# Kernel tuning notes

Measured on AMD Instinct MI355X. Metric: run time of the kernel, lower is better.

## Reference

```python
import jax, jax.numpy as jnp
import numpy as np

E = 1024   # embedding_size
K = 64     # key_size
DH = 64    # head_size
H = 16     # layer_size (num heads)
F = 4096   # hidden_size
B, S = 4, 2048
EPS = float(np.finfo(np.float32).eps)  # torch RMSNorm default eps


def setup_inputs() -> dict:
    key = jax.random.key(0)
    ks = jax.random.split(key, 12)
    embeddings = jax.random.normal(ks[0], (B, S, E), dtype=jnp.float32)
    # causal additive mask: 0 on/below diagonal, -1e9 above
    tri = jnp.triu(jnp.ones((S, S), dtype=bool), k=1)
    causal_buffer = jnp.where(tri, -1e9, 0.0).astype(jnp.float32)[None]  # [1,S,S]
    # standard RoPE cos/sin buffers over the key dim
    inv_freq = 1.0 / (10000.0 ** (jnp.arange(0, K // 2, dtype=jnp.float32) * 2.0 / K))
    ang = jnp.arange(S, dtype=jnp.float32)[:, None] * inv_freq[None, :]  # [S,K/2]
    ang = jnp.concatenate([ang, ang], axis=-1)                           # [S,K]
    cos_buffer = jnp.cos(ang)[None]  # [1,S,K]
    sin_buffer = jnp.sin(ang)[None]
    sc = 0.02
    wq = jax.random.normal(ks[1], (H, E, K), dtype=jnp.float32) * sc
    wk = jax.random.normal(ks[2], (H, E, K), dtype=jnp.float32) * sc
    wv = jax.random.normal(ks[3], (H, E, DH), dtype=jnp.float32) * sc
    w_proj = jax.random.normal(ks[4], (E, E), dtype=jnp.float32) * sc
    attn_norm_w = jnp.ones((E,), dtype=jnp.float32)
    mlp_norm_w = jnp.ones((E,), dtype=jnp.float32)
    w_up = jax.random.normal(ks[5], (E, F), dtype=jnp.float32) * sc
    w_gate = jax.random.normal(ks[6], (E, F), dtype=jnp.float32) * sc
    w_down = jax.random.normal(ks[7], (F, E), dtype=jnp.float32) * sc
    return {"embeddings": embeddings, "causal_buffer": causal_buffer,
            "cos_buffer": cos_buffer, "sin_buffer": sin_buffer,
            "wq": wq, "wk": wk, "wv": wv, "w_proj": w_proj,
            "attn_norm_w": attn_norm_w, "mlp_norm_w": mlp_norm_w,
            "w_up": w_up, "w_gate": w_gate, "w_down": w_down}


def _rmsnorm(x, w):
    ms = jnp.mean(x * x, axis=-1, keepdims=True)
    return x * jax.lax.rsqrt(ms + EPS) * w


def _rotate(x, cos, sin):
    # x: [B,H,S,K]; cos/sin: [1,1,S,K]. swapped = cat(second_half, first_half)
    swapped = jnp.concatenate([x[..., K // 2:], x[..., :K // 2]], axis=-1)
    return cos * x + sin * swapped


def reference(embeddings, causal_buffer, cos_buffer, sin_buffer,
              wq, wk, wv, w_proj, attn_norm_w, mlp_norm_w,
              w_up, w_gate, w_down):
    cos = cos_buffer[:, None]  # [1,1,S,K]
    sin = sin_buffer[:, None]
    # NOTE: original computes attention_norm(embeddings) but feeds RAW
    # embeddings to the heads; we reproduce that faithfully.
    q = _rotate(jnp.einsum('bse,hek->bhsk', embeddings, wq), cos, sin)
    k = _rotate(jnp.einsum('bse,hek->bhsk', embeddings, wk), cos, sin)
    v = jnp.einsum('bse,hed->bhsd', embeddings, wv)
    scores = jnp.einsum('bhsk,bhtk->bhst', q, k) / jnp.sqrt(jnp.float32(K))
    scores = scores + causal_buffer[:, None]  # broadcast over heads
    weights = jax.nn.softmax(scores, axis=-1)
    attn = jnp.einsum('bhst,bhtd->bhsd', weights, v)  # [B,H,S,DH]
    attn = attn.transpose(0, 2, 1, 3).reshape(attn.shape[0], attn.shape[2], H * DH)
    x = embeddings + attn @ w_proj
    h = _rmsnorm(x, mlp_norm_w)
    mlp = (h @ w_up) * jax.nn.elu(h @ w_gate)
    return x + mlp @ w_down
```

## Files before the change

### kernel.cpp

```cpp
#include <hip/hip_runtime.h>
#include <cstdint>
#include <cstddef>

#define E_DIM 1024
#define S_LEN 2048
#define NB 4
#define NH 16
#define F_DIM 4096

typedef __attribute__((ext_vector_type(8))) __bf16 bf16x8;
typedef __attribute__((ext_vector_type(4))) __bf16 bf16x4;
typedef __attribute__((ext_vector_type(4))) float f32x4;

__device__ __forceinline__ f32x4 mfma16(bf16x8 a, bf16x8 b, f32x4 c) {
  return __builtin_amdgcn_mfma_f32_16x16x32_bf16(a, b, c, 0, 0, 0);
}

__device__ __forceinline__ unsigned short f2bf(float f) {
  __bf16 h = (__bf16)f;
  return __builtin_bit_cast(unsigned short, h);
}

__device__ __forceinline__ void gl_lds16(const void* gptr, void* lptr) {
  __builtin_amdgcn_global_load_lds(
      (const __attribute__((address_space(1))) void*)gptr,
      (__attribute__((address_space(3))) void*)lptr, 16, 0, 0);
}


__global__ __launch_bounds__(256) void cast_emb_kernel(
    const float4* __restrict__ in, ushort4* __restrict__ out) {
  int i = blockIdx.x * 256 + threadIdx.x;
  float4 v = in[i];
  ushort4 o;
  o.x = f2bf(v.x); o.y = f2bf(v.y); o.z = f2bf(v.z); o.w = f2bf(v.w);
  out[i] = o;
}

__global__ __launch_bounds__(256) void transpose_cast_kernel(
    const float* __restrict__ in, unsigned short* __restrict__ out, int R, int C) {
  __shared__ float tile[32][33];
  const int bz = blockIdx.z;
  const float* ip = in + (size_t)bz * R * C;
  const int r0 = blockIdx.y * 32, c0 = blockIdx.x * 32;
  const int tc = threadIdx.x & 31, tr = threadIdx.x >> 5;
#pragma unroll
  for (int i = 0; i < 4; ++i)
    tile[tr + i * 8][tc] = ip[(size_t)(r0 + tr + i * 8) * C + (c0 + tc)];
  __syncthreads();
#pragma unroll
  for (int i = 0; i < 4; ++i)
    out[(size_t)(bz * C + c0 + tr + i * 8) * R + (r0 + tc)] = f2bf(tile[tc][tr + i * 8]);
}

template <int EPI>
__global__ __launch_bounds__(256) void gemm_bt(
    const unsigned short* __restrict__ A, const unsigned short* __restrict__ Bt,
    int Kd, int N,
    const float* __restrict__ aux, const float* __restrict__ cosb,
    const float* __restrict__ sinb,
    unsigned short* __restrict__ qout, unsigned short* __restrict__ kout,
    unsigned short* __restrict__ vtout, float* __restrict__ fout) {
  __shared__ unsigned short As[128 * 64];
  __shared__ unsigned short Bs[128 * 64];
  const int t = threadIdx.x;
  const int lane = t & 63, w = t >> 6;
  const int quad = lane >> 4, l15 = lane & 15;
  const int wm = (w >> 1) * 64, wn = (w & 1) * 64;
  const int m0 = blockIdx.y * 128, n0 = blockIdx.x * 128;
  const int sr = t >> 3, sc = t & 7;
  const int gcoff = (sc ^ (sr & 7)) * 8;
  const unsigned short* ga = A + (size_t)(m0 + sr) * Kd + gcoff;
  const unsigned short* gb = Bt + (size_t)(n0 + sr) * Kd + gcoff;
  unsigned short* lA = &As[sr * 64 + sc * 8];
  unsigned short* lB = &Bs[sr * 64 + sc * 8];
  const int xh = l15 & 7;
  f32x4 acc[4][4] = {};
  for (int k0 = 0; k0 < Kd; k0 += 64) {
    __syncthreads();
#pragma unroll
    for (int i = 0; i < 4; ++i) {
      gl_lds16(ga + (size_t)(i * 32) * Kd + k0, lA + i * 32 * 64);
      gl_lds16(gb + (size_t)(i * 32) * Kd + k0, lB + i * 32 * 64);
    }
    __syncthreads();
#pragma unroll
    for (int ks = 0; ks < 2; ++ks) {
      bf16x8 af[4], bfr[4];
#pragma unroll
      for (int mi = 0; mi < 4; ++mi)
        af[mi] = *reinterpret_cast<const bf16x8*>(
            &As[(wm + mi * 16 + l15) * 64 + (((ks * 4 + quad) ^ xh) * 8)]);
#pragma unroll
      for (int ni = 0; ni < 4; ++ni)
        bfr[ni] = *reinterpret_cast<const bf16x8*>(
            &Bs[(wn + ni * 16 + l15) * 64 + (((ks * 4 + quad) ^ xh) * 8)]);
#pragma unroll
      for (int mi = 0; mi < 4; ++mi)
#pragma unroll
        for (int ni = 0; ni < 4; ++ni)
          acc[mi][ni] = mfma16(af[mi], bfr[ni], acc[mi][ni]);
    }
  }
  if (EPI == 0) {
#pragma unroll
    for (int mi = 0; mi < 4; ++mi) {
      const int mbase = m0 + wm + mi * 16 + quad * 4;
#pragma unroll
      for (int nt = 0; nt < 4; ++nt) {
        const int n = n0 + wn + nt * 16 + l15;
        const int seg = n >> 10, rest = n & 1023, hh = rest >> 6, kk = rest & 63;
#pragma unroll
        for (int rg = 0; rg < 4; ++rg) {
          const int m = mbase + rg;
          const int b = m >> 11, s = m & 2047;
          const float v = acc[mi][nt][rg];
          if (seg == 2) {
            vtout[(((size_t)(b * NH + hh)) * 64 + kk) * S_LEN + s] = f2bf(v);
          } else {
            const float sw = acc[mi][nt ^ 2][rg];
            const float cv = cosb[s * 64 + kk], sv = sinb[s * 64 + kk];
            const float scl = (seg == 0) ? 0.125f : 1.0f;
            unsigned short* dst = (seg == 0) ? qout : kout;
            dst[(((size_t)(b * NH + hh)) * S_LEN + s) * 64 + kk] = f2bf((cv * v + sv * sw) * scl);
          }
        }
      }
    }
  } else {
#pragma unroll
    for (int mi = 0; mi < 4; ++mi) {
      const int mbase = m0 + wm + mi * 16 + quad * 4;
#pragma unroll
      for (int nt = 0; nt < 4; ++nt) {
        const int n = n0 + wn + nt * 16 + l15;
#pragma unroll
        for (int rg = 0; rg < 4; ++rg) {
          const size_t idx = (size_t)(mbase + rg) * 1024 + n;
          fout[idx] = aux[idx] + acc[mi][nt][rg];
        }
      }
    }
  }
}

__global__ __launch_bounds__(256) void gemm_upgate(
    const unsigned short* __restrict__ A, const unsigned short* __restrict__ Bu,
    const unsigned short* __restrict__ Bg, unsigned short* __restrict__ gout) {
  __shared__ unsigned short As[128 * 64];
  __shared__ unsigned short Us[64 * 64];
  __shared__ unsigned short Gs[64 * 64];
  const int Kd = 1024;
  const int t = threadIdx.x;
  const int lane = t & 63, w = t >> 6;
  const int quad = lane >> 4, l15 = lane & 15;
  const int wm = (w >> 1) * 64, wn = (w & 1) * 32;
  const int m0 = blockIdx.y * 128, n0 = blockIdx.x * 64;
  const int sr = t >> 3, sc = t & 7;
  const int gcoff = (sc ^ (sr & 7)) * 8;
  const unsigned short* ga = A + (size_t)(m0 + sr) * Kd + gcoff;
  const unsigned short* gu = Bu + (size_t)(n0 + sr) * Kd + gcoff;
  const unsigned short* gg = Bg + (size_t)(n0 + sr) * Kd + gcoff;
  unsigned short* lA = &As[sr * 64 + sc * 8];
  unsigned short* lU = &Us[sr * 64 + sc * 8];
  unsigned short* lG = &Gs[sr * 64 + sc * 8];
  const int xh = l15 & 7;
  f32x4 au[4][2] = {}, ag[4][2] = {};
  for (int k0 = 0; k0 < Kd; k0 += 64) {
    __syncthreads();
#pragma unroll
    for (int i = 0; i < 4; ++i)
      gl_lds16(ga + (size_t)(i * 32) * Kd + k0, lA + i * 32 * 64);
#pragma unroll
    for (int i = 0; i < 2; ++i) {
      gl_lds16(gu + (size_t)(i * 32) * Kd + k0, lU + i * 32 * 64);
      gl_lds16(gg + (size_t)(i * 32) * Kd + k0, lG + i * 32 * 64);
    }
    __syncthreads();
#pragma unroll
    for (int ks = 0; ks < 2; ++ks) {
      const int cp = ((ks * 4 + quad) ^ xh) * 8;
      bf16x8 af[4], bu[2], bg[2];
#pragma unroll
      for (int mi = 0; mi < 4; ++mi)
        af[mi] = *reinterpret_cast<const bf16x8*>(&As[(wm + mi * 16 + l15) * 64 + cp]);
#pragma unroll
      for (int ni = 0; ni < 2; ++ni) {
        bu[ni] = *reinterpret_cast<const bf16x8*>(&Us[(wn + ni * 16 + l15) * 64 + cp]);
        bg[ni] = *reinterpret_cast<const bf16x8*>(&Gs[(wn + ni * 16 + l15) * 64 + cp]);
      }
#pragma unroll
      for (int mi = 0; mi < 4; ++mi)
#pragma unroll
        for (int ni = 0; ni < 2; ++ni) {
          au[mi][ni] = mfma16(af[mi], bu[ni], au[mi][ni]);
          ag[mi][ni] = mfma16(af[mi], bg[ni], ag[mi][ni]);
        }
    }
  }
#pragma unroll
  for (int mi = 0; mi < 4; ++mi) {
    const int mbase = m0 + wm + mi * 16 + quad * 4;
#pragma unroll
    for (int ni = 0; ni < 2; ++ni) {
      const int n = n0 + wn + ni * 16 + l15;
#pragma unroll
      for (int rg = 0; rg < 4; ++rg) {
        const float u = au[mi][ni][rg], gt = ag[mi][ni][rg];
        const float e = gt > 0.f ? gt : (__expf(gt) - 1.f);
        gout[(size_t)(mbase + rg) * F_DIM + n] = f2bf(u * e);
      }
    }
  }
}

#define PS_STRIDE 68
__global__ __launch_bounds__(256) void flash_attn(
    const unsigned short* __restrict__ qb, const unsigned short* __restrict__ kb,
    const unsigned short* __restrict__ vtb, unsigned short* __restrict__ attn) {
  __shared__ unsigned short Ks[64 * 64];
  __shared__ unsigned short Vts[64 * 64];
  __shared__ unsigned short Ps[128 * PS_STRIDE];
  const int t = threadIdx.x, lane = t & 63, w = t >> 6;
  const int quad = lane >> 4, l15 = lane & 15;
  const int qt = 15 - blockIdx.y;
  const int bh = blockIdx.x;
  const int b = bh >> 4, hh = bh & 15;
  const unsigned short* qg = qb + (size_t)bh * S_LEN * 64;
  const unsigned short* kg = kb + (size_t)bh * S_LEN * 64;
  const unsigned short* vg = vtb + (size_t)bh * 64 * S_LEN;
  bf16x8 aq[2][2];
#pragma unroll
  for (int mi = 0; mi < 2; ++mi)
#pragma unroll
    for (int ks = 0; ks < 2; ++ks)
      aq[mi][ks] = *reinterpret_cast<const bf16x8*>(
          qg + (size_t)(qt * 128 + w * 32 + mi * 16 + l15) * 64 + ks * 32 + quad * 8);
  f32x4 o[2][4] = {};
  float lpart[2][4] = {};
  const int srk = t >> 3, sck = t & 7;
  const int gck = ((sck ^ (srk & 7)) * 8);
  const int xh = l15 & 7;
  const int ktmax = 2 * qt + 1;
  for (int kt = 0; kt <= ktmax; ++kt) {
    __syncthreads();
#pragma unroll
    for (int i = 0; i < 2; ++i) {
      gl_lds16(kg + (size_t)(kt * 64 + srk + i * 32) * 64 + gck,
               &Ks[(srk + i * 32) * 64 + sck * 8]);
      gl_lds16(vg + (size_t)(srk + i * 32) * S_LEN + kt * 64 + gck,
               &Vts[(srk + i * 32) * 64 + sck * 8]);
    }
    __syncthreads();
    f32x4 sacc[2][4];
#pragma unroll
    for (int mi = 0; mi < 2; ++mi)
#pragma unroll
      for (int nt = 0; nt < 4; ++nt) sacc[mi][nt] = (f32x4){-8.f, -8.f, -8.f, -8.f};
#pragma unroll
    for (int nt = 0; nt < 4; ++nt) {
      bf16x8 b0 = *reinterpret_cast<const bf16x8*>(
          &Ks[(nt * 16 + l15) * 64 + ((quad ^ xh) * 8)]);
      bf16x8 b1 = *reinterpret_cast<const bf16x8*>(
          &Ks[(nt * 16 + l15) * 64 + (((4 + quad) ^ xh) * 8)]);
#pragma unroll
      for (int mi = 0; mi < 2; ++mi) {
        sacc[mi][nt] = mfma16(aq[mi][0], b0, sacc[mi][nt]);
        sacc[mi][nt] = mfma16(aq[mi][1], b1, sacc[mi][nt]);
      }
    }
    if (kt >= 2 * qt) {
#pragma unroll
      for (int mi = 0; mi < 2; ++mi)
#pragma unroll
        for (int nt = 0; nt < 4; ++nt)
#pragma unroll
          for (int rg = 0; rg < 4; ++rg) {
            const int row = qt * 128 + w * 32 + mi * 16 + quad * 4 + rg;
            const int col = kt * 64 + nt * 16 + l15;
            if (col > row) sacc[mi][nt][rg] = -1e9f;
          }
    }
#pragma unroll
    for (int mi = 0; mi < 2; ++mi)
#pragma unroll
      for (int nt = 0; nt < 4; ++nt)
#pragma unroll
        for (int rg = 0; rg < 4; ++rg) {
          const float p = __expf(sacc[mi][nt][rg]);
          lpart[mi][rg] += p;
          Ps[(w * 32 + mi * 16 + quad * 4 + rg) * PS_STRIDE + nt * 16 + l15] = f2bf(p);
        }
#pragma unroll
    for (int ks = 0; ks < 2; ++ks) {
      bf16x8 ap[2];
#pragma unroll
      for (int mi = 0; mi < 2; ++mi) {
        const unsigned short* pp =
            &Ps[(w * 32 + mi * 16 + l15) * PS_STRIDE + ks * 32 + quad * 8];
        bf16x4 lo = *reinterpret_cast<const bf16x4*>(pp);
        bf16x4 hi = *reinterpret_cast<const bf16x4*>(pp + 4);
        ap[mi] = __builtin_shufflevector(lo, hi, 0, 1, 2, 3, 4, 5, 6, 7);
      }
#pragma unroll
      for (int vt = 0; vt < 4; ++vt) {
        bf16x8 bv = *reinterpret_cast<const bf16x8*>(
            &Vts[(vt * 16 + l15) * 64 + (((ks * 4 + quad) ^ xh) * 8)]);
#pragma unroll
        for (int mi = 0; mi < 2; ++mi) o[mi][vt] = mfma16(ap[mi], bv, o[mi][vt]);
      }
    }
  }
  float linv[2][4];
#pragma unroll
  for (int mi = 0; mi < 2; ++mi)
#pragma unroll
    for (int rg = 0; rg < 4; ++rg) {
      float rs = lpart[mi][rg];
#pragma unroll
      for (int d = 1; d < 16; d <<= 1) rs += __shfl_xor(rs, d);
      linv[mi][rg] = 1.0f / rs;
    }
#pragma unroll
  for (int mi = 0; mi < 2; ++mi)
#pragma unroll
    for (int vt = 0; vt < 4; ++vt)
#pragma unroll
      for (int rg = 0; rg < 4; ++rg) {
        const int row = w * 32 + mi * 16 + quad * 4 + rg;
        const int s = qt * 128 + row;
        const float ov = o[mi][vt][rg] * linv[mi][rg];
        attn[((size_t)(b * S_LEN + s)) * E_DIM + hh * 64 + vt * 16 + l15] = f2bf(ov);
      }
}

__global__ __launch_bounds__(256) void rmsnorm_kernel(
    const float* __restrict__ x, const float* __restrict__ wgt,
    unsigned short* __restrict__ hout) {
  const int row = blockIdx.x;
  const int t = threadIdx.x;
  const float4 v = reinterpret_cast<const float4*>(x + (size_t)row * E_DIM)[t];
  float ss = v.x * v.x + v.y * v.y + v.z * v.z + v.w * v.w;
#pragma unroll
  for (int d = 1; d < 64; d <<= 1) ss += __shfl_xor(ss, d);
  __shared__ float red[4];
  if ((t & 63) == 0) red[t >> 6] = ss;
  __syncthreads();
  const float tot = red[0] + red[1] + red[2] + red[3];
  const float sc = rsqrtf(tot * (1.f / 1024.f) + 1.1920929e-07f);
  const float4 g = reinterpret_cast<const float4*>(wgt)[t];
  ushort4 ov;
  ov.x = f2bf(v.x * sc * g.x);
  ov.y = f2bf(v.y * sc * g.y);
  ov.z = f2bf(v.z * sc * g.z);
  ov.w = f2bf(v.w * sc * g.w);
  reinterpret_cast<ushort4*>(hout + (size_t)row * E_DIM)[t] = ov;
}

extern "C" void kernel_launch(void* const* d_in, const int* in_sizes, int n_in,
                              void* d_out, int out_size, void* d_ws, size_t ws_size,
                              hipStream_t stream) {
  (void)in_sizes; (void)n_in; (void)out_size; (void)ws_size;
  const float* emb = (const float*)d_in[0];
  const float* cosb = (const float*)d_in[2];
  const float* sinb = (const float*)d_in[3];
  const float* wq = (const float*)d_in[4];
  const float* wk = (const float*)d_in[5];
  const float* wv = (const float*)d_in[6];
  const float* wproj = (const float*)d_in[7];
  const float* mlpw = (const float*)d_in[9];
  const float* wup = (const float*)d_in[10];
  const float* wgate = (const float*)d_in[11];
  const float* wdown = (const float*)d_in[12];
  float* out = (float*)d_out;
  char* ws = (char*)d_ws;
  unsigned short* wqkv_t = (unsigned short*)(ws + 0);
  unsigned short* wproj_t = (unsigned short*)(ws + 6291456);
  unsigned short* wup_t = (unsigned short*)(ws + 8388608);
  unsigned short* wgate_t = (unsigned short*)(ws + 16777216);
  unsigned short* wdown_t = (unsigned short*)(ws + 25165824);
  unsigned short* embb = (unsigned short*)(ws + 33554432);
  unsigned short* qbuf = (unsigned short*)(ws + 50331648);
  unsigned short* kbuf = (unsigned short*)(ws + 67108864);
  unsigned short* vtbuf = (unsigned short*)(ws + 83886080);
  unsigned short* gbuf = (unsigned short*)(ws + 33554432);
  unsigned short* attnb = (unsigned short*)(ws + 100663296);
  float* xbuf = (float*)(ws + 117440512);
  unsigned short* hbuf = (unsigned short*)(ws + 150994944);

  dim3 blk(256);
  cast_emb_kernel<<<8192, blk, 0, stream>>>((const float4*)emb, (ushort4*)embb);
  transpose_cast_kernel<<<dim3(2, 32, 16), blk, 0, stream>>>(wq, wqkv_t, 1024, 64);
  transpose_cast_kernel<<<dim3(2, 32, 16), blk, 0, stream>>>(wk, wqkv_t + 1024 * 1024, 1024, 64);
  transpose_cast_kernel<<<dim3(2, 32, 16), blk, 0, stream>>>(wv, wqkv_t + 2048 * 1024, 1024, 64);
  transpose_cast_kernel<<<dim3(32, 32, 1), blk, 0, stream>>>(wproj, wproj_t, 1024, 1024);
  transpose_cast_kernel<<<dim3(128, 32, 1), blk, 0, stream>>>(wup, wup_t, 1024, 4096);
  transpose_cast_kernel<<<dim3(128, 32, 1), blk, 0, stream>>>(wgate, wgate_t, 1024, 4096);
  transpose_cast_kernel<<<dim3(32, 128, 1), blk, 0, stream>>>(wdown, wdown_t, 4096, 1024);
  gemm_bt<0><<<dim3(24, 64), blk, 0, stream>>>(embb, wqkv_t, 1024, 3072, nullptr, cosb,
                                               sinb, qbuf, kbuf, vtbuf, nullptr);
  flash_attn<<<dim3(64, 16), blk, 0, stream>>>(qbuf, kbuf, vtbuf, attnb);
  gemm_bt<1><<<dim3(8, 64), blk, 0, stream>>>(attnb, wproj_t, 1024, 1024, emb, nullptr,
                                              nullptr, nullptr, nullptr, nullptr, xbuf);
  rmsnorm_kernel<<<8192, blk, 0, stream>>>(xbuf, mlpw, hbuf);
  gemm_upgate<<<dim3(64, 64), blk, 0, stream>>>(hbuf, wup_t, wgate_t, gbuf);
  gemm_bt<2><<<dim3(8, 64), blk, 0, stream>>>(gbuf, wdown_t, 4096, 1024, xbuf, nullptr,
                                              nullptr, nullptr, nullptr, nullptr, out);
}
```

Measured before the change: 639.4 us.

## Double-buffer B tiles, load A fragments directly from global, interleave up/gate weights

The GEMM kernel now loads A-operand fragments straight from global memory into registers, prefetched one K-step ahead, instead of staging them through LDS. B tiles are double-buffered in LDS so the next tile loads while the current one is used, leaving one barrier per iteration. The up and gate weights are transposed into one interleaved matrix in 16-row groups, so the up/gate GEMM reuses the generic kernel with an ELU-gating epilogue on adjacent accumulator tiles. K is now a template parameter. The trade-off is more registers and uncoalesced, non-LDS-shared A reads: each wave fetches its own rows, and the two waves sharing an M range fetch the same A data twice.

```diff
diff --git a/kernel.cpp b/kernel.cpp
--- a/kernel.cpp
+++ b/kernel.cpp
@@ -38,7 +38,8 @@
 }
 
 __global__ __launch_bounds__(256) void transpose_cast_kernel(
-    const float* __restrict__ in, unsigned short* __restrict__ out, int R, int C) {
+    const float* __restrict__ in, unsigned short* __restrict__ out, int R, int C,
+    int mode) {
   __shared__ float tile[32][33];
   const int bz = blockIdx.z;
   const float* ip = in + (size_t)bz * R * C;
@@ -49,20 +50,23 @@
     tile[tr + i * 8][tc] = ip[(size_t)(r0 + tr + i * 8) * C + (c0 + tc)];
   __syncthreads();
 #pragma unroll
-  for (int i = 0; i < 4; ++i)
-    out[(size_t)(bz * C + c0 + tr + i * 8) * R + (r0 + tc)] = f2bf(tile[tc][tr + i * 8]);
-}
-
-template <int EPI>
+  for (int i = 0; i < 4; ++i) {
+    const int c = c0 + tr + i * 8;
+    const int row = (mode == 0) ? (bz * C + c)
+                                : (32 * (c >> 4) + (c & 15) + (mode == 2 ? 16 : 0));
+    out[(size_t)row * R + (r0 + tc)] = f2bf(tile[tc][tr + i * 8]);
+  }
+}
+
+template <int EPI, int KD>
 __global__ __launch_bounds__(256) void gemm_bt(
     const unsigned short* __restrict__ A, const unsigned short* __restrict__ Bt,
-    int Kd, int N,
     const float* __restrict__ aux, const float* __restrict__ cosb,
     const float* __restrict__ sinb,
     unsigned short* __restrict__ qout, unsigned short* __restrict__ kout,
-    unsigned short* __restrict__ vtout, float* __restrict__ fout) {
-  __shared__ unsigned short As[128 * 64];
-  __shared__ unsigned short Bs[128 * 64];
+    unsigned short* __restrict__ vtout, float* __restrict__ fout,
+    unsigned short* __restrict__ gout) {
+  __shared__ unsigned short Bs[2][128 * 64];
   const int t = threadIdx.x;
   const int lane = t & 63, w = t >> 6;
   const int quad = lane >> 4, l15 = lane & 15;
@@ -70,37 +74,54 @@
   const int m0 = blockIdx.y * 128, n0 = blockIdx.x * 128;
   const int sr = t >> 3, sc = t & 7;
   const int gcoff = (sc ^ (sr & 7)) * 8;
-  const unsigned short* ga = A + (size_t)(m0 + sr) * Kd + gcoff;
-  const unsigned short* gb = Bt + (size_t)(n0 + sr) * Kd + gcoff;
-  unsigned short* lA = &As[sr * 64 + sc * 8];
-  unsigned short* lB = &Bs[sr * 64 + sc * 8];
+  const unsigned short* gb = Bt + (size_t)(n0 + sr) * KD + gcoff;
   const int xh = l15 & 7;
+  const unsigned short* ga = A + (size_t)(m0 + wm + l15) * KD + quad * 8;
   f32x4 acc[4][4] = {};
-  for (int k0 = 0; k0 < Kd; k0 += 64) {
-    __syncthreads();
-#pragma unroll
-    for (int i = 0; i < 4; ++i) {
-      gl_lds16(ga + (size_t)(i * 32) * Kd + k0, lA + i * 32 * 64);
-      gl_lds16(gb + (size_t)(i * 32) * Kd + k0, lB + i * 32 * 64);
-    }
-    __syncthreads();
+  bf16x8 afc[2][4], afn[2][4];
+#pragma unroll
+  for (int i = 0; i < 4; ++i)
+    gl_lds16(gb + (size_t)(i * 32) * KD, &Bs[0][(sr + i * 32) * 64 + sc * 8]);
+#pragma unroll
+  for (int ks = 0; ks < 2; ++ks)
+#pragma unroll
+    for (int mi = 0; mi < 4; ++mi)
+      afc[ks][mi] =
+          *reinterpret_cast<const bf16x8*>(ga + (size_t)(mi * 16) * KD + ks * 32);
+  __syncthreads();
+#pragma unroll 2
+  for (int k0 = 0; k0 < KD; k0 += 64) {
+    const int cur = (k0 >> 6) & 1;
+    if (k0 + 64 < KD) {
+#pragma unroll
+      for (int i = 0; i < 4; ++i)
+        gl_lds16(gb + (size_t)(i * 32) * KD + k0 + 64,
+                 &Bs[cur ^ 1][(sr + i * 32) * 64 + sc * 8]);
+#pragma unroll
+      for (int ks = 0; ks < 2; ++ks)
+#pragma unroll
+        for (int mi = 0; mi < 4; ++mi)
+          afn[ks][mi] = *reinterpret_cast<const bf16x8*>(
+              ga + (size_t)(mi * 16) * KD + k0 + 64 + ks * 32);
+    }
 #pragma unroll
     for (int ks = 0; ks < 2; ++ks) {
-      bf16x8 af[4], bfr[4];
-#pragma unroll
-      for (int mi = 0; mi < 4; ++mi)
-        af[mi] = *reinterpret_cast<const bf16x8*>(
-            &As[(wm + mi * 16 + l15) * 64 + (((ks * 4 + quad) ^ xh) * 8)]);
+      bf16x8 bfr[4];
 #pragma unroll
       for (int ni = 0; ni < 4; ++ni)
         bfr[ni] = *reinterpret_cast<const bf16x8*>(
-            &Bs[(wn + ni * 16 + l15) * 64 + (((ks * 4 + quad) ^ xh) * 8)]);
+            &Bs[cur][(wn + ni * 16 + l15) * 64 + (((ks * 4 + quad) ^ xh) * 8)]);
 #pragma unroll
       for (int mi = 0; mi < 4; ++mi)
 #pragma unroll
         for (int ni = 0; ni < 4; ++ni)
-          acc[mi][ni] = mfma16(af[mi], bfr[ni], acc[mi][ni]);
-    }
+          acc[mi][ni] = mfma16(afc[ks][mi], bfr[ni], acc[mi][ni]);
+    }
+    __syncthreads();
+#pragma unroll
+    for (int ks = 0; ks < 2; ++ks)
+#pragma unroll
+      for (int mi = 0; mi < 4; ++mi) afc[ks][mi] = afn[ks][mi];
   }
   if (EPI == 0) {
 #pragma unroll
@@ -122,8 +143,24 @@
             const float cv = cosb[s * 64 + kk], sv = sinb[s * 64 + kk];
             const float scl = (seg == 0) ? 0.125f : 1.0f;
             unsigned short* dst = (seg == 0) ? qout : kout;
-            dst[(((size_t)(b * NH + hh)) * S_LEN + s) * 64 + kk] = f2bf((cv * v + sv * sw) * scl);
+            dst[(((size_t)(b * NH + hh)) * S_LEN + s) * 64 + kk] =
+                f2bf((cv * v + sv * sw) * scl);
           }
+        }
+      }
+    }
+  } else if (EPI == 3) {
+#pragma unroll
+    for (int mi = 0; mi < 4; ++mi) {
+      const int mbase = m0 + wm + mi * 16 + quad * 4;
+#pragma unroll
+      for (int nt = 0; nt < 4; nt += 2) {
+        const int col = (n0 >> 1) + (wn >> 1) + (nt >> 1) * 16 + l15;
+#pragma unroll
+        for (int rg = 0; rg < 4; ++rg) {
+          const float u = acc[mi][nt][rg], gt = acc[mi][nt + 1][rg];
+          const float e = gt > 0.f ? gt : (__expf(gt) - 1.f);
+          gout[(size_t)(mbase + rg) * F_DIM + col] = f2bf(u * e);
         }
       }
     }
@@ -139,76 +176,6 @@
           const size_t idx = (size_t)(mbase + rg) * 1024 + n;
           fout[idx] = aux[idx] + acc[mi][nt][rg];
         }
-      }
-    }
-  }
-}
-
-__global__ __launch_bounds__(256) void gemm_upgate(
-    const unsigned short* __restrict__ A, const unsigned short* __restrict__ Bu,
-    const unsigned short* __restrict__ Bg, unsigned short* __restrict__ gout) {
-  __shared__ unsigned short As[128 * 64];
-  __shared__ unsigned short Us[64 * 64];
-  __shared__ unsigned short Gs[64 * 64];
-  const int Kd = 1024;
-  const int t = threadIdx.x;
-  const int lane = t & 63, w = t >> 6;
-  const int quad = lane >> 4, l15 = lane & 15;
-  const int wm = (w >> 1) * 64, wn = (w & 1) * 32;
-  const int m0 = blockIdx.y * 128, n0 = blockIdx.x * 64;
-  const int sr = t >> 3, sc = t & 7;
-  const int gcoff = (sc ^ (sr & 7)) * 8;
-  const unsigned short* ga = A + (size_t)(m0 + sr) * Kd + gcoff;
-  const unsigned short* gu = Bu + (size_t)(n0 + sr) * Kd + gcoff;
-  const unsigned short* gg = Bg + (size_t)(n0 + sr) * Kd + gcoff;
-  unsigned short* lA = &As[sr * 64 + sc * 8];
-  unsigned short* lU = &Us[sr * 64 + sc * 8];
-  unsigned short* lG = &Gs[sr * 64 + sc * 8];
-  const int xh = l15 & 7;
-  f32x4 au[4][2] = {}, ag[4][2] = {};
-  for (int k0 = 0; k0 < Kd; k0 += 64) {
-    __syncthreads();
-#pragma unroll
-    for (int i = 0; i < 4; ++i)
-      gl_lds16(ga + (size_t)(i * 32) * Kd + k0, lA + i * 32 * 64);
-#pragma unroll
-    for (int i = 0; i < 2; ++i) {
-      gl_lds16(gu + (size_t)(i * 32) * Kd + k0, lU + i * 32 * 64);
-      gl_lds16(gg + (size_t)(i * 32) * Kd + k0, lG + i * 32 * 64);
-    }
-    __syncthreads();
-#pragma unroll
-    for (int ks = 0; ks < 2; ++ks) {
-      const int cp = ((ks * 4 + quad) ^ xh) * 8;
-      bf16x8 af[4], bu[2], bg[2];
-#pragma unroll
-      for (int mi = 0; mi < 4; ++mi)
-        af[mi] = *reinterpret_cast<const bf16x8*>(&As[(wm + mi * 16 + l15) * 64 + cp]);
-#pragma unroll
-      for (int ni = 0; ni < 2; ++ni) {
-        bu[ni] = *reinterpret_cast<const bf16x8*>(&Us[(wn + ni * 16 + l15) * 64 + cp]);
-        bg[ni] = *reinterpret_cast<const bf16x8*>(&Gs[(wn + ni * 16 + l15) * 64 + cp]);
-      }
-#pragma unroll
-      for (int mi = 0; mi < 4; ++mi)
-#pragma unroll
-        for (int ni = 0; ni < 2; ++ni) {
-          au[mi][ni] = mfma16(af[mi], bu[ni], au[mi][ni]);
-          ag[mi][ni] = mfma16(af[mi], bg[ni], ag[mi][ni]);
-        }
-    }
-  }
-#pragma unroll
-  for (int mi = 0; mi < 4; ++mi) {
-    const int mbase = m0 + wm + mi * 16 + quad * 4;
-#pragma unroll
-    for (int ni = 0; ni < 2; ++ni) {
-      const int n = n0 + wn + ni * 16 + l15;
-#pragma unroll
-      for (int rg = 0; rg < 4; ++rg) {
-        const float u = au[mi][ni][rg], gt = ag[mi][ni][rg];
-        const float e = gt > 0.f ? gt : (__expf(gt) - 1.f);
-        gout[(size_t)(mbase + rg) * F_DIM + n] = f2bf(u * e);
       }
     }
   }
@@ -376,8 +343,7 @@
   char* ws = (char*)d_ws;
   unsigned short* wqkv_t = (unsigned short*)(ws + 0);
   unsigned short* wproj_t = (unsigned short*)(ws + 6291456);
-  unsigned short* wup_t = (unsigned short*)(ws + 8388608);
-  unsigned short* wgate_t = (unsigned short*)(ws + 16777216);
+  unsigned short* wupgate_t = (unsigned short*)(ws + 8388608);
   unsigned short* wdown_t = (unsigned short*)(ws + 25165824);
   unsigned short* embb = (unsigned short*)(ws + 33554432);
   unsigned short* qbuf = (unsigned short*)(ws + 50331648);
@@ -390,20 +356,21 @@
 
   dim3 blk(256);
   cast_emb_kernel<<<8192, blk, 0, stream>>>((const float4*)emb, (ushort4*)embb);
-  transpose_cast_kernel<<<dim3(2, 32, 16), blk, 0, stream>>>(wq, wqkv_t, 1024, 64);
-  transpose_cast_kernel<<<dim3(2, 32, 16), blk, 0, stream>>>(wk, wqkv_t + 1024 * 1024, 1024, 64);
-  transpose_cast_kernel<<<dim3(2, 32, 16), blk, 0, stream>>>(wv, wqkv_t + 2048 * 1024, 1024, 64);
-  transpose_cast_kernel<<<dim3(32, 32, 1), blk, 0, stream>>>(wproj, wproj_t, 1024, 1024);
-  transpose_cast_kernel<<<dim3(128, 32, 1), blk, 0, stream>>>(wup, wup_t, 1024, 4096);
-  transpose_cast_kernel<<<dim3(128, 32, 1), blk, 0, stream>>>(wgate, wgate_t, 1024, 4096);
-  transpose_cast_kernel<<<dim3(32, 128, 1), blk, 0, stream>>>(wdown, wdown_t, 4096, 1024);
-  gemm_bt<0><<<dim3(24, 64), blk, 0, stream>>>(embb, wqkv_t, 1024, 3072, nullptr, cosb,
-                                               sinb, qbuf, kbuf, vtbuf, nullptr);
+  transpose_cast_kernel<<<dim3(2, 32, 16), blk, 0, stream>>>(wq, wqkv_t, 1024, 64, 0);
+  transpose_cast_kernel<<<dim3(2, 32, 16), blk, 0, stream>>>(wk, wqkv_t + 1024 * 1024, 1024, 64, 0);
+  transpose_cast_kernel<<<dim3(2, 32, 16), blk, 0, stream>>>(wv, wqkv_t + 2048 * 1024, 1024, 64, 0);
+  transpose_cast_kernel<<<dim3(32, 32, 1), blk, 0, stream>>>(wproj, wproj_t, 1024, 1024, 0);
+  transpose_cast_kernel<<<dim3(128, 32, 1), blk, 0, stream>>>(wup, wupgate_t, 1024, 4096, 1);
+  transpose_cast_kernel<<<dim3(128, 32, 1), blk, 0, stream>>>(wgate, wupgate_t, 1024, 4096, 2);
+  transpose_cast_kernel<<<dim3(32, 128, 1), blk, 0, stream>>>(wdown, wdown_t, 4096, 1024, 0);
+  gemm_bt<0, 1024><<<dim3(24, 64), blk, 0, stream>>>(
+      embb, wqkv_t, nullptr, cosb, sinb, qbuf, kbuf, vtbuf, nullptr, nullptr);
   flash_attn<<<dim3(64, 16), blk, 0, stream>>>(qbuf, kbuf, vtbuf, attnb);
-  gemm_bt<1><<<dim3(8, 64), blk, 0, stream>>>(attnb, wproj_t, 1024, 1024, emb, nullptr,
-                                              nullptr, nullptr, nullptr, nullptr, xbuf);
+  gemm_bt<1, 1024><<<dim3(8, 64), blk, 0, stream>>>(
+      attnb, wproj_t, emb, nullptr, nullptr, nullptr, nullptr, nullptr, xbuf, nullptr);
   rmsnorm_kernel<<<8192, blk, 0, stream>>>(xbuf, mlpw, hbuf);
-  gemm_upgate<<<dim3(64, 64), blk, 0, stream>>>(hbuf, wup_t, wgate_t, gbuf);
-  gemm_bt<2><<<dim3(8, 64), blk, 0, stream>>>(gbuf, wdown_t, 4096, 1024, xbuf, nullptr,
-                                              nullptr, nullptr, nullptr, nullptr, out);
-}
+  gemm_bt<3, 1024><<<dim3(64, 64), blk, 0, stream>>>(
+      hbuf, wupgate_t, nullptr, nullptr, nullptr, nullptr, nullptr, nullptr, nullptr, gbuf);
+  gemm_bt<2, 4096><<<dim3(8, 64), blk, 0, stream>>>(
+      gbuf, wdown_t, xbuf, nullptr, nullptr, nullptr, nullptr, nullptr, out, nullptr);
+}
```

Result: slower. 929.3 us (+45.3%).
